# Optimization experiments

Hardware: AMD Instinct MI355X
Metric: run time of the kernel (lower is better)

## Reference

```python
import jax, jax.numpy as jnp
import numpy as np

N_E = 16384
E_DIM = 256
BETA = 0.25


def setup_inputs() -> dict:
    key = jax.random.key(0)
    k1, k2 = jax.random.split(key)
    z = jax.random.normal(k1, (8, E_DIM, 32, 32), dtype=jnp.float32)
    embedding = jax.random.uniform(
        k2, (N_E, E_DIM), dtype=jnp.float32, minval=-1.0 / N_E, maxval=1.0 / N_E
    )
    return {"z": z, "embedding": embedding}


def reference(z, embedding):
    # b c h w -> b h w c
    zc = jnp.transpose(z, (0, 2, 3, 1))
    b, h, w, c = zc.shape
    z_flat = zc.reshape(-1, c)  # [N, e_dim]

    # squared-distance matrix: ||z||^2 + ||e||^2 - 2 z e^T  -> [N, n_e]
    d = (
        jnp.sum(z_flat * z_flat, axis=1, keepdims=True)
        + jnp.sum(embedding * embedding, axis=1)
        - 2.0 * jnp.einsum("nd,kd->nk", z_flat, embedding)
    )
    idx = jnp.argmin(d, axis=1)  # [N]

    z_q = embedding[idx].reshape(b, h, w, c)

    sg = jax.lax.stop_gradient
    # legacy=True loss: mse(sg(z_q), z) + beta * mse(z_q, sg(z))
    loss = jnp.mean((sg(z_q) - zc) ** 2) + BETA * jnp.mean((z_q - sg(zc)) ** 2)

    # straight-through estimator
    z_q_st = zc + sg(z_q - zc)
    z_q_out = jnp.transpose(z_q_st, (0, 3, 1, 2))  # b h w c -> b c h w
    return z_q_out, loss, idx
```

## Files before the change

kernel.cpp:

```cpp
#include <hip/hip_runtime.h>

#define E_DIM  256
#define N_E    16384
#define N_ROWS 8192
#define HW     1024
#define NPART  128

typedef _Float16 f16x8 __attribute__((ext_vector_type(8)));
typedef float    f32x4 __attribute__((ext_vector_type(4)));

#define ESCALE   1048576.0f
#define UNSCALE  1.9073486328125e-6f

#define ROR_DPP(v, CTRL) \
  ((unsigned)__builtin_amdgcn_update_dpp(0, (int)(v), (CTRL), 0xF, 0xF, false))

__device__ __forceinline__ float score_ref32(const float* zr,
                                             const float* __restrict__ E,
                                             const float* __restrict__ eNorm,
                                             int idx, float zn) {
  const float4* e4p = (const float4*)(E + (size_t)idx * E_DIM);
  float d0 = 0.f, d1 = 0.f, d2 = 0.f, d3 = 0.f;
#pragma unroll 16
  for (int q = 0; q < 64; ++q) {
    float4 e4 = e4p[q];
    d0 = fmaf(zr[q * 4 + 0], e4.x, d0);
    d1 = fmaf(zr[q * 4 + 1], e4.y, d1);
    d2 = fmaf(zr[q * 4 + 2], e4.z, d2);
    d3 = fmaf(zr[q * 4 + 3], e4.w, d3);
  }
  float dot = (d0 + d1) + (d2 + d3);
  float base = zn + eNorm[idx];
  float td = 2.0f * dot;
  return base - td;
}

#define ZB_Z    256
#define EB_E    512
__global__ __launch_bounds__(256) void k_prep(const float* __restrict__ z,
                                              const float* __restrict__ E,
                                              _Float16* __restrict__ Ah,
                                              _Float16* __restrict__ Bh,
                                              float* __restrict__ eNorm,
                                              float* __restrict__ zNorm,
                                              float* __restrict__ zL1,
                                              float* __restrict__ out_loss) {
#pragma clang fp contract(off)
  const int bi = blockIdx.x, t = threadIdx.x;

  if (bi < ZB_Z) {
    __shared__ float sLZ[256][32];
    __shared__ float sN2[16][32];
    __shared__ float sL1[16][32];
    const int n0 = bi * 32;
    const int b = n0 >> 10, hw0 = n0 & 1023;

    {
      const int nl = t & 31, cs = t >> 5;
      const float* zb = z + (size_t)b * E_DIM * HW + hw0 + nl;
#pragma unroll 4
      for (int it = 0; it < 32; ++it) {
        int c = it * 8 + cs;
        sLZ[c][nl] = zb[(size_t)c * HW];
      }
    }
    __syncthreads();

    {
      const int nl = t & 31, seg = t >> 5;
      const int n = n0 + nl;
      const int perm = (n >> 1) & 3;
#pragma unroll
      for (int u = 0; u < 4; ++u) {
        const int c0 = seg * 32 + u * 8;
        f16x8 hh;
#pragma unroll
        for (int j = 0; j < 8; ++j) hh[j] = (_Float16)sLZ[c0 + j][nl];
        size_t dst = (size_t)seg * (N_ROWS * 32) + (size_t)n * 32 + (size_t)(u ^ perm) * 8;
        *(f16x8*)&Ah[dst] = hh;
      }
    }

#pragma unroll
    for (int it = 0; it < 2; ++it) {
      int task = it * 256 + t;
      int nl = task & 31, c16 = task >> 5;
      int h = c16 >> 3, j = c16 & 7;
      float r2 = 0.f, r1 = 0.f;
#pragma unroll
      for (int i = 0; i < 16; ++i) {
        float v = sLZ[h * 128 + i * 8 + j][nl];
        r2 = r2 + v * v;
        r1 = r1 + fabsf(v);
      }
      sN2[c16][nl] = r2;
      sL1[c16][nl] = r1;
    }
    __syncthreads();
    if (t < 32) {
      float q[16], p[16];
#pragma unroll
      for (int c16 = 0; c16 < 16; ++c16) { q[c16] = sN2[c16][t]; p[c16] = sL1[c16][t]; }
      float h0 = ((q[0] + q[1]) + (q[2] + q[3])) + ((q[4] + q[5]) + (q[6] + q[7]));
      float h1 = ((q[8] + q[9]) + (q[10] + q[11])) + ((q[12] + q[13]) + (q[14] + q[15]));
      zNorm[n0 + t] = h0 + h1;
      float g0 = ((p[0] + p[1]) + (p[2] + p[3])) + ((p[4] + p[5]) + (p[6] + p[7]));
      float g1 = ((p[8] + p[9]) + (p[10] + p[11])) + ((p[12] + p[13]) + (p[14] + p[15]));
      zL1[n0 + t] = g0 + g1;
    }
  } else {
    __shared__ float sNP[8][32];
    const int be = bi - ZB_Z;
    if (be == 0 && t == 0) out_loss[0] = 0.f;
    const int kc = t >> 5, rl = t & 31;
    const int k = be * 32 + rl;
    const int perm = (k >> 1) & 3;
    const float* src = E + (size_t)k * E_DIM + kc * 32;

    float4 v4[8];
#pragma unroll
    for (int u2 = 0; u2 < 8; ++u2) v4[u2] = ((const float4*)src)[u2];

    float nsum = 0.f;
    size_t base = (size_t)kc * (N_E * 32) + (size_t)k * 32;
#pragma unroll
    for (int u = 0; u < 4; ++u) {
      float v[8] = {v4[u * 2].x, v4[u * 2].y, v4[u * 2].z, v4[u * 2].w,
                    v4[u * 2 + 1].x, v4[u * 2 + 1].y, v4[u * 2 + 1].z, v4[u * 2 + 1].w};
      f16x8 hh;
#pragma unroll
      for (int j = 0; j < 8; ++j) {
        nsum = nsum + v[j] * v[j];
        hh[j] = (_Float16)(v[j] * ESCALE);
      }
      *(f16x8*)&Bh[base + (size_t)(u ^ perm) * 8] = hh;
    }
    sNP[kc][rl] = nsum;
    __syncthreads();
    if (t < 32) {
      float s = 0.f;
#pragma unroll
      for (int kc2 = 0; kc2 < 8; ++kc2) s += sNP[kc2][t];
      eNorm[be * 32 + t] = s;
    }
  }
}

__global__ __launch_bounds__(256, 2) void k_scores_mfma(
    const _Float16* __restrict__ Ah, const _Float16* __restrict__ Bh,
    const float* __restrict__ eNorm,
    unsigned* __restrict__ pK1, unsigned* __restrict__ pK2,
    unsigned* __restrict__ pK3) {
#pragma clang fp contract(off)
  __shared__ float eNq[128];
  __shared__ unsigned sK1[256];
  __shared__ unsigned sK2[256];
  __shared__ unsigned sK3[256];

  const int mt = blockIdx.x, nt = blockIdx.y;
  const int m0 = mt * 128, n0 = nt * 128;

  const int t = threadIdx.x;
  const int lane = t & 63, w = t >> 6;
  const int tx = lane & 15, quad = lane >> 4;
  const int wr = w & 1, wc = w >> 1;
  const int wm = wr * 64, wn = wc * 64;
  const int swz = (quad ^ ((tx >> 1) & 3)) * 8;

  const size_t planeA = (size_t)N_ROWS * 32, planeB = (size_t)N_E * 32;
  const size_t baseA = (size_t)(m0 + wm + tx) * 32 + swz;
  const size_t baseB = (size_t)(n0 + wn + tx) * 32 + swz;

  if (t < 128) eNq[t] = fmaf(eNorm[n0 + t], 2097152.f, 131072.f);

  f32x4 acc[4][4];
#pragma unroll
  for (int i = 0; i < 4; ++i)
#pragma unroll
    for (int j = 0; j < 4; ++j) acc[i][j] = (f32x4){0.f, 0.f, 0.f, 0.f};

#pragma unroll
  for (int kc = 0; kc < 8; ++kc) {
    f16x8 ah[4], bh[4];
#pragma unroll
    for (int i = 0; i < 4; ++i)
      ah[i] = *(const f16x8*)&Ah[kc * planeA + baseA + (size_t)i * 512];
#pragma unroll
    for (int j = 0; j < 4; ++j)
      bh[j] = *(const f16x8*)&Bh[kc * planeB + baseB + (size_t)j * 512];

    __builtin_amdgcn_s_setprio(1);
#pragma unroll
    for (int j = 0; j < 4; ++j)
#pragma unroll
      for (int i = 0; i < 4; ++i)
        acc[i][j] = __builtin_amdgcn_mfma_f32_16x16x32_f16(ah[i], bh[j], acc[i][j], 0, 0, 0);
    __builtin_amdgcn_s_setprio(0);
  }

  __syncthreads();

#pragma unroll
  for (int i = 0; i < 4; ++i) {
#pragma unroll
    for (int r = 0; r < 4; ++r) {
      const int rloc = wm + i * 16 + quad * 4 + r;
      unsigned k0, k1, k2, k3;
      {
        float tq0 = fmaf(acc[i][0][r], -4.0f, eNq[wn + 0 * 16 + tx]);
        float tq1 = fmaf(acc[i][1][r], -4.0f, eNq[wn + 1 * 16 + tx]);
        float tq2 = fmaf(acc[i][2][r], -4.0f, eNq[wn + 2 * 16 + tx]);
        float tq3 = fmaf(acc[i][3][r], -4.0f, eNq[wn + 3 * 16 + tx]);
        k0 = (((unsigned)tq0) << 14) | (unsigned)(n0 + wn + 0 * 16 + tx);
        k1 = (((unsigned)tq1) << 14) | (unsigned)(n0 + wn + 1 * 16 + tx);
        k2 = (((unsigned)tq2) << 14) | (unsigned)(n0 + wn + 2 * 16 + tx);
        k3 = (((unsigned)tq3) << 14) | (unsigned)(n0 + wn + 3 * 16 + tx);
      }
      unsigned a = min(k0, k1), b = max(k0, k1);
      unsigned c = min(k2, k3), d = max(k2, k3);
      unsigned m1 = min(a, c), e = max(a, c);
      unsigned f = min(b, d);
      unsigned m2 = min(e, f), m3 = max(e, f);
#define MERGE_R(CTRL)                                              \
      {                                                            \
        unsigned o1 = ROR_DPP(m1, CTRL);                           \
        unsigned o2 = ROR_DPP(m2, CTRL);                           \
        unsigned o3 = ROR_DPP(m3, CTRL);                           \
        unsigned n1 = min(m1, o1);                                 \
        unsigned n2 = min(max(m1, o1), min(m2, o2));               \
        unsigned n3 = min(min(m3, o3), min(max(m2, o1), max(m1, o2))); \
        m1 = n1; m2 = n2; m3 = n3;                                 \
      }
      MERGE_R(0x121)
      MERGE_R(0x122)
      MERGE_R(0x124)
      MERGE_R(0x128)
#undef MERGE_R
      if (tx == 0) {
        sK1[wc * 128 + rloc] = m1;
        sK2[wc * 128 + rloc] = m2;
        sK3[wc * 128 + rloc] = m3;
      }
    }
  }
  __syncthreads();
  if (t < 128) {
    unsigned a1 = sK1[t], a2 = sK2[t], a3 = sK3[t];
    unsigned b1 = sK1[128 + t], b2 = sK2[128 + t], b3 = sK3[128 + t];
    const size_t o = (size_t)nt * N_ROWS + m0 + t;
    pK1[o] = min(a1, b1);
    pK2[o] = min(max(a1, b1), min(a2, b2));
    pK3[o] = min(min(a3, b3), min(max(a2, b1), max(a1, b2)));
  }
}

__global__ __launch_bounds__(1024) void k_post(
    const unsigned* __restrict__ pK1, const unsigned* __restrict__ pK2,
    const unsigned* __restrict__ pK3,
    const float* __restrict__ zL1, const float* __restrict__ zNorm,
    const float* __restrict__ z, const float* __restrict__ E,
    const float* __restrict__ eNorm,
    float* __restrict__ out, float* __restrict__ out_loss,
    float* __restrict__ out_idx) {
#pragma clang fp contract(off)
  __shared__ float zc[32][264];
  __shared__ unsigned sM[32][32];
  __shared__ unsigned gK[32];
  __shared__ int   fI[32];
  __shared__ int   cand[32][16];
  __shared__ int   ccnt[32];
  __shared__ int   heavy[32][4];
  __shared__ int   hcnt[32];
  __shared__ float fS[32][32];
  __shared__ int   fiS[32][32];
  __shared__ float wsum[16];

  const int t = threadIdx.x;
  const int r = t & 31, s = t >> 5;
  const int n0 = blockIdx.x * 32;
  const int n = n0 + r;
  const int b = n >> 10, hw = n & 1023;

  if (t < 32) { ccnt[t] = 0; hcnt[t] = 0; }

  {
    const float* zrow = z + ((size_t)b * E_DIM + s * 8) * HW + hw;
#pragma unroll
    for (int k = 0; k < 8; ++k) zc[r][s * 8 + k] = zrow[(size_t)k * HW];
  }

  unsigned mk = 0xFFFFFFFFu;
#pragma unroll
  for (int i = 0; i < 4; ++i) {
    int ti = s * 4 + i;
    mk = min(mk, pK1[(size_t)ti * N_ROWS + n]);
  }
  sM[s][r] = mk;
  __syncthreads();
  if (t < 32) {
    unsigned bk = sM[0][t];
#pragma unroll
    for (int s3 = 1; s3 < 32; ++s3) bk = min(bk, sM[s3][t]);
    gK[t] = bk;
  }
  __syncthreads();

  {
    const unsigned qW =
        (unsigned)(fmaf(zL1[n], 2.384185791015625e-7f, 8e-5f) * 2097152.f) + 3u;
    unsigned thrq = (gK[r] >> 14) + qW;
    if (thrq > 262143u) thrq = 262143u;
    const unsigned thrk = (thrq << 14) | 0x3FFFu;
#pragma unroll
    for (int i = 0; i < 4; ++i) {
      int ti = s * 4 + i;
      size_t o = (size_t)ti * N_ROWS + n;
      unsigned k1 = pK1[o], k2 = pK2[o], k3 = pK3[o];
      if (k1 <= thrk) { int p = atomicAdd(&ccnt[r], 1); if (p < 16) cand[r][p] = (int)(k1 & 0x3FFFu); }
      if (k2 <= thrk) { int p = atomicAdd(&ccnt[r], 1); if (p < 16) cand[r][p] = (int)(k2 & 0x3FFFu); }
      if (k3 <= thrk) { int p = atomicAdd(&hcnt[r], 1); if (p < 4)  heavy[r][p] = ti; }
    }
  }
  __syncthreads();

  {
    const int rcnt = ccnt[r], rhc = hcnt[r];
    const bool ovf = (rcnt > 16) || (rhc > 4);
    const bool ex = (rcnt > 1) || (rhc > 0);
    float bv = 3.4e38f;
    int bi = 0x7fffffff;
    if (ex) {
      const float zn = zNorm[n];
      if (ovf) {
        for (int k = s; k < N_E; k += 32) {
          float sp = score_ref32(&zc[r][0], E, eNorm, k, zn);
          if (sp < bv || (sp == bv && k < bi)) { bv = sp; bi = k; }
        }
      } else {
        for (int c = s; c < rcnt; c += 32) {
          int idx = cand[r][c];
          float sp = score_ref32(&zc[r][0], E, eNorm, idx, zn);
          if (sp < bv || (sp == bv && idx < bi)) { bv = sp; bi = idx; }
        }
        for (int h = 0; h < rhc; ++h) {
          int ti = heavy[r][h];
          for (int cc = s; cc < 128; cc += 32) {
            int idx = ti * 128 + cc;
            float sp = score_ref32(&zc[r][0], E, eNorm, idx, zn);
            if (sp < bv || (sp == bv && idx < bi)) { bv = sp; bi = idx; }
          }
        }
      }
    }
    fS[r][s] = bv;
    fiS[r][s] = bi;
  }
  __syncthreads();
  if (t < 32) {
    const int rcnt = ccnt[t], rhc = hcnt[t];
    int fidx;
    if (rcnt <= 1 && rhc == 0) {
      fidx = (int)(gK[t] & 0x3FFFu);
    } else {
      float bv = fS[t][0];
      int bi = fiS[t][0];
#pragma unroll
      for (int s3 = 1; s3 < 32; ++s3) {
        float v = fS[t][s3];
        int id = fiS[t][s3];
        if (v < bv || (v == bv && id < bi)) { bv = v; bi = id; }
      }
      fidx = bi;
    }
    fI[t] = fidx;
    out_idx[n0 + t] = (float)fidx;
  }
  __syncthreads();

  const int idx = fI[r];
  const float4* erow4 = (const float4*)(E + (size_t)idx * E_DIM + s * 8);
  float* orow = out + ((size_t)b * E_DIM + s * 8) * HW + hw;
  float acc = 0.f;
#pragma unroll
  for (int c4 = 0; c4 < 2; ++c4) {
    float4 e4 = erow4[c4];
    float ev[4] = {e4.x, e4.y, e4.z, e4.w};
#pragma unroll
    for (int j2 = 0; j2 < 4; ++j2) {
      int c = c4 * 4 + j2;
      float zv = zc[r][s * 8 + c];
      orow[(size_t)c * HW] = ev[j2];
      float d = ev[j2] - zv;
      acc = fmaf(d, d, acc);
    }
  }
  for (int off = 32; off > 0; off >>= 1) acc += __shfl_down(acc, off, 64);
  if ((t & 63) == 0) wsum[t >> 6] = acc;
  __syncthreads();
  if (t == 0) {
    float s0 = 0.f;
#pragma unroll
    for (int wv = 0; wv < 16; ++wv) s0 += wsum[wv];
    atomicAdd(out_loss, s0 * (1.25f / 2097152.f));
  }
}

extern "C" void kernel_launch(void* const* d_in, const int* in_sizes, int n_in,
                              void* d_out, int out_size, void* d_ws, size_t ws_size,
                              hipStream_t stream) {
  const float* z = (const float*)d_in[0];
  const float* E = (const float*)d_in[1];
  float* out = (float*)d_out;
  float* out_loss = out + 2097152;
  float* out_idx = out + 2097153;

  _Float16* Ah = (_Float16*)d_ws;
  _Float16* Bh = Ah + (size_t)N_ROWS * E_DIM;
  float* eNorm = (float*)(Bh + (size_t)N_E * E_DIM);
  float* zL1 = eNorm + N_E;
  float* zNorm = zL1 + N_ROWS;
  unsigned* pK1 = (unsigned*)(zNorm + N_ROWS);
  unsigned* pK2 = pK1 + (size_t)NPART * N_ROWS;
  unsigned* pK3 = pK2 + (size_t)NPART * N_ROWS;

  k_prep<<<ZB_Z + EB_E, 256, 0, stream>>>(z, E, Ah, Bh, eNorm, zNorm, zL1, out_loss);
  k_scores_mfma<<<dim3(N_ROWS / 128, N_E / 128), 256, 0, stream>>>(
      Ah, Bh, eNorm, pK1, pK2, pK3);
  k_post<<<N_ROWS / 32, 1024, 0, stream>>>(
      pK1, pK2, pK3, zL1, zNorm, z, E, eNorm, out, out_loss, out_idx);
}
```

Baseline: 183.4 us.

## Use 2 waves per block with 64x128 warp tiles, drop LDS cross-wave merge

```diff
diff --git a/kernel.cpp b/kernel.cpp
--- a/kernel.cpp
+++ b/kernel.cpp
@@ -146,81 +146,77 @@
   }
 }
 
-__global__ __launch_bounds__(256, 2) void k_scores_mfma(
+__global__ __launch_bounds__(128, 2) void k_scores_mfma(
     const _Float16* __restrict__ Ah, const _Float16* __restrict__ Bh,
     const float* __restrict__ eNorm,
     unsigned* __restrict__ pK1, unsigned* __restrict__ pK2,
     unsigned* __restrict__ pK3) {
 #pragma clang fp contract(off)
-  __shared__ float eNq[128];
-  __shared__ unsigned sK1[256];
-  __shared__ unsigned sK2[256];
-  __shared__ unsigned sK3[256];
-
   const int mt = blockIdx.x, nt = blockIdx.y;
   const int m0 = mt * 128, n0 = nt * 128;
 
   const int t = threadIdx.x;
   const int lane = t & 63, w = t >> 6;
   const int tx = lane & 15, quad = lane >> 4;
-  const int wr = w & 1, wc = w >> 1;
-  const int wm = wr * 64, wn = wc * 64;
+  const int wm = w * 64;
   const int swz = (quad ^ ((tx >> 1) & 3)) * 8;
 
   const size_t planeA = (size_t)N_ROWS * 32, planeB = (size_t)N_E * 32;
   const size_t baseA = (size_t)(m0 + wm + tx) * 32 + swz;
-  const size_t baseB = (size_t)(n0 + wn + tx) * 32 + swz;
-
-  if (t < 128) eNq[t] = fmaf(eNorm[n0 + t], 2097152.f, 131072.f);
-
-  f32x4 acc[4][4];
+  const size_t baseB = (size_t)(n0 + tx) * 32 + swz;
+
+  f32x4 acc[4][8];
 #pragma unroll
   for (int i = 0; i < 4; ++i)
 #pragma unroll
-    for (int j = 0; j < 4; ++j) acc[i][j] = (f32x4){0.f, 0.f, 0.f, 0.f};
+    for (int j = 0; j < 8; ++j) acc[i][j] = (f32x4){0.f, 0.f, 0.f, 0.f};
 
 #pragma unroll
   for (int kc = 0; kc < 8; ++kc) {
-    f16x8 ah[4], bh[4];
+    f16x8 ah[4], bh[8];
 #pragma unroll
     for (int i = 0; i < 4; ++i)
       ah[i] = *(const f16x8*)&Ah[kc * planeA + baseA + (size_t)i * 512];
 #pragma unroll
-    for (int j = 0; j < 4; ++j)
+    for (int j = 0; j < 8; ++j)
       bh[j] = *(const f16x8*)&Bh[kc * planeB + baseB + (size_t)j * 512];
 
     __builtin_amdgcn_s_setprio(1);
 #pragma unroll
-    for (int j = 0; j < 4; ++j)
+    for (int j = 0; j < 8; ++j)
 #pragma unroll
       for (int i = 0; i < 4; ++i)
         acc[i][j] = __builtin_amdgcn_mfma_f32_16x16x32_f16(ah[i], bh[j], acc[i][j], 0, 0, 0);
     __builtin_amdgcn_s_setprio(0);
   }
 
-  __syncthreads();
+  float enq[8];
+#pragma unroll
+  for (int j = 0; j < 8; ++j)
+    enq[j] = fmaf(eNorm[n0 + j * 16 + tx], 2097152.f, 131072.f);
 
 #pragma unroll
   for (int i = 0; i < 4; ++i) {
 #pragma unroll
     for (int r = 0; r < 4; ++r) {
       const int rloc = wm + i * 16 + quad * 4 + r;
-      unsigned k0, k1, k2, k3;
-      {
-        float tq0 = fmaf(acc[i][0][r], -4.0f, eNq[wn + 0 * 16 + tx]);
-        float tq1 = fmaf(acc[i][1][r], -4.0f, eNq[wn + 1 * 16 + tx]);
-        float tq2 = fmaf(acc[i][2][r], -4.0f, eNq[wn + 2 * 16 + tx]);
-        float tq3 = fmaf(acc[i][3][r], -4.0f, eNq[wn + 3 * 16 + tx]);
-        k0 = (((unsigned)tq0) << 14) | (unsigned)(n0 + wn + 0 * 16 + tx);
-        k1 = (((unsigned)tq1) << 14) | (unsigned)(n0 + wn + 1 * 16 + tx);
-        k2 = (((unsigned)tq2) << 14) | (unsigned)(n0 + wn + 2 * 16 + tx);
-        k3 = (((unsigned)tq3) << 14) | (unsigned)(n0 + wn + 3 * 16 + tx);
-      }
-      unsigned a = min(k0, k1), b = max(k0, k1);
-      unsigned c = min(k2, k3), d = max(k2, k3);
-      unsigned m1 = min(a, c), e = max(a, c);
-      unsigned f = min(b, d);
-      unsigned m2 = min(e, f), m3 = max(e, f);
+      unsigned k[8];
+#pragma unroll
+      for (int j = 0; j < 8; ++j) {
+        float tq = fmaf(acc[i][j][r], -4.0f, enq[j]);
+        k[j] = (((unsigned)tq) << 14) | (unsigned)(n0 + j * 16 + tx);
+      }
+      unsigned a = min(k[0], k[1]), b = max(k[0], k[1]);
+      unsigned c = min(k[2], k[3]), d = max(k[2], k[3]);
+      unsigned a1 = min(a, c), e0 = max(a, c), f0 = min(b, d);
+      unsigned a2 = min(e0, f0), a3 = max(e0, f0);
+      a = min(k[4], k[5]); b = max(k[4], k[5]);
+      c = min(k[6], k[7]); d = max(k[6], k[7]);
+      unsigned b1 = min(a, c); e0 = max(a, c); f0 = min(b, d);
+      unsigned b2 = min(e0, f0), b3 = max(e0, f0);
+      unsigned m1 = min(a1, b1);
+      unsigned m2 = min(max(a1, b1), min(a2, b2));
+      unsigned m3 = min(min(a3, b3), min(max(a2, b1), max(a1, b2)));
 #define MERGE_R(CTRL)                                              \
       {                                                            \
         unsigned o1 = ROR_DPP(m1, CTRL);                           \
@@ -237,20 +233,12 @@
       MERGE_R(0x128)
 #undef MERGE_R
       if (tx == 0) {
-        sK1[wc * 128 + rloc] = m1;
-        sK2[wc * 128 + rloc] = m2;
-        sK3[wc * 128 + rloc] = m3;
-      }
-    }
-  }
-  __syncthreads();
-  if (t < 128) {
-    unsigned a1 = sK1[t], a2 = sK2[t], a3 = sK3[t];
-    unsigned b1 = sK1[128 + t], b2 = sK2[128 + t], b3 = sK3[128 + t];
-    const size_t o = (size_t)nt * N_ROWS + m0 + t;
-    pK1[o] = min(a1, b1);
-    pK2[o] = min(max(a1, b1), min(a2, b2));
-    pK3[o] = min(min(a3, b3), min(max(a2, b1), max(a1, b2)));
+        const size_t o = (size_t)nt * N_ROWS + m0 + rloc;
+        pK1[o] = m1;
+        pK2[o] = m2;
+        pK3[o] = m3;
+      }
+    }
   }
 }
 
@@ -424,7 +412,7 @@
   unsigned* pK3 = pK2 + (size_t)NPART * N_ROWS;
 
   k_prep<<<ZB_Z + EB_E, 256, 0, stream>>>(z, E, Ah, Bh, eNorm, zNorm, zL1, out_loss);
-  k_scores_mfma<<<dim3(N_ROWS / 128, N_E / 128), 256, 0, stream>>>(
+  k_scores_mfma<<<dim3(N_ROWS / 128, N_E / 128), 128, 0, stream>>>(
       Ah, Bh, eNorm, pK1, pK2, pK3);
   k_post<<<N_ROWS / 32, 1024, 0, stream>>>(
       pK1, pK2, pK3, zL1, zNorm, z, E, eNorm, out, out_loss, out_idx);
```

Result: faster. 176.8 us (-3.6%).
